# Performance work log

Hardware: AMD Instinct MI355X
Metric: run time of the kernel (lower is better)

The kernel has to match this reference:

```python
import jax, jax.numpy as jnp
import numpy as np


def setup_inputs() -> dict:
    key = jax.random.key(0)
    ks = jax.random.split(key, 8)
    B, N = 4, 256
    E, C, H = 64, 128, 256
    return {
        "edge_features": jax.random.normal(ks[0], (B, E, N, N), dtype=jnp.float32),
        "node_features": jax.random.normal(ks[1], (B, C, N), dtype=jnp.float32),
        "W1": jax.random.normal(ks[2], (H, E + 2 * C), dtype=jnp.float32) * 0.05,
        "b1": jax.random.normal(ks[3], (H,), dtype=jnp.float32) * 0.05,
        "W2": jax.random.normal(ks[4], (H, H), dtype=jnp.float32) * 0.05,
        "b2": jax.random.normal(ks[5], (H,), dtype=jnp.float32) * 0.05,
        "W3": jax.random.normal(ks[6], (1, H), dtype=jnp.float32) * 0.05,
        "b3": jax.random.normal(ks[7], (1,), dtype=jnp.float32) * 0.05,
    }


def reference(edge_features, node_features, W1, b1, W2, b2, W3, b3):
    B, C, N = node_features.shape
    # node_addon_row: [B, C, N, N] broadcast along last dim; col along dim 2
    row = jnp.broadcast_to(node_features[:, :, :, None], (B, C, N, N))
    col = jnp.broadcast_to(node_features[:, :, None, :], (B, C, N, N))
    x = jnp.concatenate([edge_features, row, col], axis=1)  # [B, E+2C, N, N]
    # 1x1 conv == channel matmul
    x = jax.nn.relu(jnp.einsum('bcnm,oc->bonm', x, W1) + b1[None, :, None, None])
    x = jax.nn.relu(jnp.einsum('bcnm,oc->bonm', x, W2) + b2[None, :, None, None])
    x = jnp.einsum('bcnm,oc->bonm', x, W3) + b3[None, :, None, None]  # [B,1,N,N]
    return x[:, 0, :, :]
```

## Files before the change

### kernel.cpp

```cpp
#include <hip/hip_runtime.h>
#include <stdint.h>

typedef __bf16 bf16x8 __attribute__((ext_vector_type(8)));
typedef __bf16 bf16x4v __attribute__((ext_vector_type(4)));
typedef float  f32x16 __attribute__((ext_vector_type(16)));
typedef float  f32x4t __attribute__((ext_vector_type(4)));
typedef unsigned int u32x2 __attribute__((ext_vector_type(2)));

#define WS_W1S 0
#define WS_W2S 32768
#define WS_R   163840
#define WS_CT  1212416

__global__ void prep_weights(const float* __restrict__ W1, const float* __restrict__ W2,
                             __bf16* __restrict__ w1s, __bf16* __restrict__ w2s) {
    int t = blockIdx.x * 256 + threadIdx.x;
    int chunk = t >> 6, lane = t & 63;
    if (chunk < 128) {
        int wid = chunk >> 5, ks = (chunk >> 1) & 15, mb = chunk & 1;
        int o = wid * 64 + mb * 32 + (lane & 31);
        int k = ks * 16 + (lane >> 5) * 8;
        const float* src = W2 + o * 256 + k;
        __bf16* dst = w2s + chunk * 512 + lane * 8;
#pragma unroll
        for (int j = 0; j < 8; ++j) dst[j] = (__bf16)src[j];
    } else if (chunk < 160) {
        int c1 = chunk - 128;
        int wid = c1 >> 3, ks = (c1 >> 1) & 3, mb = c1 & 1;
        int o = wid * 64 + mb * 32 + (lane & 31);
        int k = ks * 16 + (lane >> 5) * 8;
        const float* src = W1 + o * 320 + k;
        __bf16* dst = w1s + c1 * 512 + lane * 8;
#pragma unroll
        for (int j = 0; j < 8; ++j) dst[j] = (__bf16)src[j];
    }
}

__global__ __launch_bounds__(256) void prep_rc(
    const float* __restrict__ W1, const float* __restrict__ b1,
    const float* __restrict__ node, float* __restrict__ Rt,
    __bf16* __restrict__ Ctb) {
    __shared__ float nds[128 * 16];
    const int b = blockIdx.x >> 4, j0 = (blockIdx.x & 15) * 16;
    const int o = threadIdx.x;
    {
        int c = threadIdx.x >> 1, jh = (threadIdx.x & 1) * 8;
        const float* src = node + b * 32768 + c * 256 + j0 + jh;
        *(float4*)&nds[c * 16 + jh] = *(const float4*)src;
        *(float4*)&nds[c * 16 + jh + 4] = *(const float4*)(src + 4);
    }
    __syncthreads();
    float aR[16], aC[16];
#pragma unroll
    for (int j = 0; j < 16; ++j) { aR[j] = 0.f; aC[j] = 0.f; }
    const float* wr = W1 + o * 320 + 64;
    const float* wc = W1 + o * 320 + 192;
    for (int c4 = 0; c4 < 32; ++c4) {
        float4 wrv = *(const float4*)(wr + c4 * 4);
        float4 wcv = *(const float4*)(wc + c4 * 4);
        const float* wrp = (const float*)&wrv;
        const float* wcp = (const float*)&wcv;
#pragma unroll
        for (int r = 0; r < 4; ++r) {
            const f32x4t* nrow = (const f32x4t*)&nds[(c4 * 4 + r) * 16];
            f32x4t n0 = nrow[0], n1 = nrow[1], n2 = nrow[2], n3 = nrow[3];
#pragma unroll
            for (int q = 0; q < 4; ++q) {
                aR[q]      = fmaf(wrp[r], n0[q], aR[q]);
                aR[q + 4]  = fmaf(wrp[r], n1[q], aR[q + 4]);
                aR[q + 8]  = fmaf(wrp[r], n2[q], aR[q + 8]);
                aR[q + 12] = fmaf(wrp[r], n3[q], aR[q + 12]);
                aC[q]      = fmaf(wcp[r], n0[q], aC[q]);
                aC[q + 4]  = fmaf(wcp[r], n1[q], aC[q + 4]);
                aC[q + 8]  = fmaf(wcp[r], n2[q], aC[q + 8]);
                aC[q + 12] = fmaf(wcp[r], n3[q], aC[q + 12]);
            }
        }
    }
    float bb = b1[o];
#pragma unroll
    for (int j = 0; j < 16; ++j) {
        int idx = ((b * 256 + j0 + j) << 8) + o;
        Rt[idx] = aR[j] + bb;
        Ctb[idx] = (__bf16)aC[j];
    }
}

__device__ inline void zero_acc(f32x16 acc[2][2]) {
#pragma unroll
    for (int i = 0; i < 2; ++i)
#pragma unroll
        for (int j = 0; j < 2; ++j)
#pragma unroll
            for (int k = 0; k < 16; ++k) acc[i][j][k] = 0.f;
}

__global__ __launch_bounds__(256, 2) void fused_main(
    const float* __restrict__ edge, const __bf16* __restrict__ w1s,
    const __bf16* __restrict__ w2s, const float* __restrict__ Rt,
    const __bf16* __restrict__ Ctb, const float* __restrict__ b2,
    const float* __restrict__ W3, const float* __restrict__ b3,
    float* __restrict__ out) {
    __shared__ unsigned int lds_e[64 * 33];
    __shared__ unsigned int lds_h1[64 * 140];
    __shared__ float lds_p[64 * 9];
    __shared__ float lds_c[512];

    const int tid = threadIdx.x;
    const int wid = tid >> 6;
    const int lane = tid & 63;
    const int p31 = lane & 31;
    const int hi = lane >> 5;
    const int obase = wid * 64;

    const int blk = blockIdx.x;
    const int b   = blk >> 7;
    const int m0  = ((blk >> 5) & 3) << 6;
    const int n0  = (blk & 31) << 3;

    lds_c[tid] = b2[tid];
    lds_c[256 + tid] = W3[tid];

    const float4* eg = (const float4*)edge;
    const int a_ = tid & 15;
    const int epb = tid >> 4;
    float4 pf[4];

#define PREFETCH(nn)                                                        \
    {                                                                       \
        _Pragma("unroll")                                                   \
        for (int r = 0; r < 2; ++r) {                                       \
            int ep = r * 16 + epb;                                          \
            int f4 = (b * 64 + ep * 2) * 16384 + (nn) * 64 + (m0 >> 2) + a_;\
            pf[r * 2]     = eg[f4];                                         \
            pf[r * 2 + 1] = eg[f4 + 16384];                                 \
        }                                                                   \
    }

#define LOAD_Q(bf, q)                                                       \
    {                                                                       \
        _Pragma("unroll")                                                   \
        for (int ksl = 0; ksl < 4; ++ksl)                                   \
            _Pragma("unroll")                                               \
            for (int mb = 0; mb < 2; ++mb)                                  \
                A2q[bf][ksl][mb] = *(const bf16x8*)(w2_s +                  \
                    ((((wid << 4) + (q) * 4 + ksl) << 1) + mb) * 512 + (lane << 3)); \
    }

    PREFETCH(n0);

    bf16x4v CvR[8][2];
#pragma unroll
    for (int mb = 0; mb < 2; ++mb)
#pragma unroll
        for (int rg = 0; rg < 4; ++rg)
#pragma unroll
            for (int nb = 0; nb < 2; ++nb)
                CvR[mb * 4 + rg][nb] = *(const bf16x4v*)(Ctb +
                    ((b * 256 + m0 + nb * 32 + p31) << 8) + obase + mb * 32 + 8 * rg + 4 * hi);

    f32x16 acc[2][2];
    bf16x8 A2q[2][4][2];
    for (int it = 0; it < 8; ++it) {
        const int n = n0 + it;

        uint64_t w1a = (uint64_t)w1s;
        asm volatile("" : "+s"(w1a));
        const __bf16* w1_s = (const __bf16*)w1a;
        uint64_t w2a = (uint64_t)w2s;
        asm volatile("" : "+s"(w2a));
        const __bf16* w2_s = (const __bf16*)w2a;

#pragma unroll
        for (int r = 0; r < 2; ++r) {
            int ep = r * 16 + epb;
            const float* p0 = (const float*)&pf[r * 2];
            const float* p1 = (const float*)&pf[r * 2 + 1];
#pragma unroll
            for (int i = 0; i < 4; ++i) {
                union { __bf16 h[2]; unsigned int u; } t;
                t.h[0] = (__bf16)p0[i];
                t.h[1] = (__bf16)p1[i];
                lds_e[(a_ * 4 + i) * 33 + ep] = t.u;
            }
        }
        bf16x8 A1[2][4];
#pragma unroll
        for (int mb = 0; mb < 2; ++mb)
#pragma unroll
            for (int ks = 0; ks < 4; ++ks)
                A1[mb][ks] = *(const bf16x8*)(w1_s +
                    ((((wid << 2) + ks) << 1) + mb) * 512 + (lane << 3));
        __syncthreads();

        zero_acc(acc);
#pragma unroll
        for (int ks = 0; ks < 4; ++ks) {
            bf16x8 B1[2];
#pragma unroll
            for (int nb = 0; nb < 2; ++nb) {
                union { unsigned int u[4]; bf16x8 v; } bb;
#pragma unroll
                for (int j = 0; j < 4; ++j)
                    bb.u[j] = lds_e[(nb * 32 + p31) * 33 + ks * 8 + hi * 4 + j];
                B1[nb] = bb.v;
            }
#pragma unroll
            for (int mb = 0; mb < 2; ++mb) {
                acc[mb][0] = __builtin_amdgcn_mfma_f32_32x32x16_bf16(A1[mb][ks], B1[0], acc[mb][0], 0, 0, 0);
                acc[mb][1] = __builtin_amdgcn_mfma_f32_32x32x16_bf16(A1[mb][ks], B1[1], acc[mb][1], 0, 0, 0);
            }
        }

        const int nRow = (b * 256 + n) << 8;
#pragma unroll
        for (int mb = 0; mb < 2; ++mb) {
#pragma unroll
            for (int rg = 0; rg < 4; ++rg) {
                int och = obase + mb * 32 + 8 * rg + 4 * hi;
                f32x4t Rv = *(const f32x4t*)(Rt + nRow + och);
#pragma unroll
                for (int nb = 0; nb < 2; ++nb) {
                    int pix = nb * 32 + p31;
                    bf16x4v Cv = CvR[mb * 4 + rg][nb];
                    union { __bf16 h[4]; u32x2 u; } t;
#pragma unroll
                    for (int rr = 0; rr < 4; ++rr) {
                        float v = acc[mb][nb][rg * 4 + rr] + Rv[rr] + (float)Cv[rr];
                        t.h[rr] = (__bf16)fmaxf(v, 0.f);
                    }
                    *(u32x2*)&lds_h1[pix * 140 + (och >> 1)] = t.u;
                }
            }
        }
        LOAD_Q(0, 0);
        if (it < 7) PREFETCH(n + 1);
        __syncthreads();

        zero_acc(acc);
#pragma unroll
        for (int q = 0; q < 4; ++q) {
            if (q < 3) LOAD_Q((q + 1) & 1, q + 1);
#pragma unroll
            for (int ksl = 0; ksl < 4; ++ksl) {
                const int ksg = q * 4 + ksl;
                bf16x8 B2[2];
#pragma unroll
                for (int nb = 0; nb < 2; ++nb)
                    B2[nb] = *(const bf16x8*)&lds_h1[(nb * 32 + p31) * 140 + ksg * 8 + hi * 4];
#pragma unroll
                for (int mb = 0; mb < 2; ++mb) {
                    acc[mb][0] = __builtin_amdgcn_mfma_f32_32x32x16_bf16(A2q[q & 1][ksl][mb], B2[0], acc[mb][0], 0, 0, 0);
                    acc[mb][1] = __builtin_amdgcn_mfma_f32_32x32x16_bf16(A2q[q & 1][ksl][mb], B2[1], acc[mb][1], 0, 0, 0);
                }
            }
        }

        float part0 = 0.f, part1 = 0.f;
#pragma unroll
        for (int mb = 0; mb < 2; ++mb) {
#pragma unroll
            for (int rg = 0; rg < 4; ++rg) {
                int och = obase + mb * 32 + 8 * rg + 4 * hi;
                f32x4t b2v = *(const f32x4t*)&lds_c[och];
                f32x4t w3v = *(const f32x4t*)&lds_c[256 + och];
#pragma unroll
                for (int rr = 0; rr < 4; ++rr) {
                    float h0 = fmaxf(acc[mb][0][rg * 4 + rr] + b2v[rr], 0.f);
                    float h1v = fmaxf(acc[mb][1][rg * 4 + rr] + b2v[rr], 0.f);
                    part0 = fmaf(w3v[rr], h0, part0);
                    part1 = fmaf(w3v[rr], h1v, part1);
                }
            }
        }
        lds_p[(0 * 32 + p31) * 9 + wid * 2 + hi] = part0;
        lds_p[(1 * 32 + p31) * 9 + wid * 2 + hi] = part1;
        __syncthreads();

        if (tid < 64) {
            float s = b3[0];
#pragma unroll
            for (int k = 0; k < 8; ++k) s += lds_p[tid * 9 + k];
            out[((b * 256 + n) << 8) + m0 + tid] = s;
        }
    }
#undef PREFETCH
#undef LOAD_Q
}

extern "C" void kernel_launch(void* const* d_in, const int* in_sizes, int n_in,
                              void* d_out, int out_size, void* d_ws, size_t ws_size,
                              hipStream_t stream) {
    const float* edge = (const float*)d_in[0];
    const float* node = (const float*)d_in[1];
    const float* W1   = (const float*)d_in[2];
    const float* b1   = (const float*)d_in[3];
    const float* W2   = (const float*)d_in[4];
    const float* b2   = (const float*)d_in[5];
    const float* W3   = (const float*)d_in[6];
    const float* b3   = (const float*)d_in[7];
    char* ws = (char*)d_ws;
    __bf16* w1s = (__bf16*)(ws + WS_W1S);
    __bf16* w2s = (__bf16*)(ws + WS_W2S);
    float*  Rt  = (float*)(ws + WS_R);
    __bf16* Ctb = (__bf16*)(ws + WS_CT);

    prep_weights<<<40, 256, 0, stream>>>(W1, W2, w1s, w2s);
    prep_rc<<<64, 256, 0, stream>>>(W1, b1, node, Rt, Ctb);
    fused_main<<<512, 256, 0, stream>>>(edge, w1s, w2s, Rt, Ctb, b2, W3, b3, (float*)d_out);
}
```

Measured before the change: 160.2 us.

## Merge prep kernels, swizzle h1 LDS, hoist W1 fragments, defer output reduction

Merges the two prep kernels into one launch and writes the column term in a fragment-contiguous layout, so the main kernel loads it with coalesced lane-strided reads. The padded h1 LDS tile is replaced by an XOR-swizzled 512-byte-row layout to avoid bank conflicts while using less LDS. W1 fragments are hoisted out of the pixel loop, the per-row R vector is staged through LDS, and the final output reduction is deferred into the next iteration to drop one barrier wait. The trade-off is more live registers and an extra barrier between layers.

```diff
diff --git a/kernel.cpp b/kernel.cpp
--- a/kernel.cpp
+++ b/kernel.cpp
@@ -12,34 +12,34 @@
 #define WS_R   163840
 #define WS_CT  1212416
 
-__global__ void prep_weights(const float* __restrict__ W1, const float* __restrict__ W2,
-                             __bf16* __restrict__ w1s, __bf16* __restrict__ w2s) {
-    int t = blockIdx.x * 256 + threadIdx.x;
-    int chunk = t >> 6, lane = t & 63;
-    if (chunk < 128) {
-        int wid = chunk >> 5, ks = (chunk >> 1) & 15, mb = chunk & 1;
-        int o = wid * 64 + mb * 32 + (lane & 31);
-        int k = ks * 16 + (lane >> 5) * 8;
-        const float* src = W2 + o * 256 + k;
-        __bf16* dst = w2s + chunk * 512 + lane * 8;
-#pragma unroll
-        for (int j = 0; j < 8; ++j) dst[j] = (__bf16)src[j];
-    } else if (chunk < 160) {
-        int c1 = chunk - 128;
-        int wid = c1 >> 3, ks = (c1 >> 1) & 3, mb = c1 & 1;
-        int o = wid * 64 + mb * 32 + (lane & 31);
-        int k = ks * 16 + (lane >> 5) * 8;
-        const float* src = W1 + o * 320 + k;
-        __bf16* dst = w1s + c1 * 512 + lane * 8;
-#pragma unroll
-        for (int j = 0; j < 8; ++j) dst[j] = (__bf16)src[j];
-    }
-}
-
-__global__ __launch_bounds__(256) void prep_rc(
+__global__ __launch_bounds__(256) void prep_all(
     const float* __restrict__ W1, const float* __restrict__ b1,
-    const float* __restrict__ node, float* __restrict__ Rt,
-    __bf16* __restrict__ Ctb) {
+    const float* __restrict__ node, const float* __restrict__ W2,
+    float* __restrict__ Rt, __bf16* __restrict__ Cts,
+    __bf16* __restrict__ w1s, __bf16* __restrict__ w2s) {
+    if (blockIdx.x >= 64) {
+        int t = (blockIdx.x - 64) * 256 + threadIdx.x;
+        int chunk = t >> 6, lane = t & 63;
+        if (chunk < 128) {
+            int wid = chunk >> 5, ks = (chunk >> 1) & 15, mb = chunk & 1;
+            int o = wid * 64 + mb * 32 + (lane & 31);
+            int k = ks * 16 + (lane >> 5) * 8;
+            const float* src = W2 + o * 256 + k;
+            __bf16* dst = w2s + chunk * 512 + lane * 8;
+#pragma unroll
+            for (int j = 0; j < 8; ++j) dst[j] = (__bf16)src[j];
+        } else if (chunk < 160) {
+            int c1 = chunk - 128;
+            int wid = c1 >> 3, ks = (c1 >> 1) & 3, mb = c1 & 1;
+            int o = wid * 64 + mb * 32 + (lane & 31);
+            int k = ks * 16 + (lane >> 5) * 8;
+            const float* src = W1 + o * 320 + k;
+            __bf16* dst = w1s + c1 * 512 + lane * 8;
+#pragma unroll
+            for (int j = 0; j < 8; ++j) dst[j] = (__bf16)src[j];
+        }
+        return;
+    }
     __shared__ float nds[128 * 16];
     const int b = blockIdx.x >> 4, j0 = (blockIdx.x & 15) * 16;
     const int o = threadIdx.x;
@@ -78,33 +78,30 @@
         }
     }
     float bb = b1[o];
+    const int wid = o >> 6, mb = (o >> 5) & 1, rg = (o >> 3) & 3;
+    const int hi = (o >> 2) & 1, oq = o & 3;
 #pragma unroll
     for (int j = 0; j < 16; ++j) {
-        int idx = ((b * 256 + j0 + j) << 8) + o;
-        Rt[idx] = aR[j] + bb;
-        Ctb[idx] = (__bf16)aC[j];
-    }
-}
-
-__device__ inline void zero_acc(f32x16 acc[2][2]) {
-#pragma unroll
-    for (int i = 0; i < 2; ++i)
-#pragma unroll
-        for (int j = 0; j < 2; ++j)
-#pragma unroll
-            for (int k = 0; k < 16; ++k) acc[i][j][k] = 0.f;
+        int m = j0 + j;
+        Rt[((b * 256 + m) << 8) + o] = aR[j] + bb;
+        int mg = m >> 6, nbm = (m >> 5) & 1, p31m = m & 31;
+        int chunk = ((((b * 4 + mg) * 4 + wid) * 2 + mb) * 4 + rg) * 2 + nbm;
+        Cts[chunk * 256 + (hi * 32 + p31m) * 4 + oq] = (__bf16)aC[j];
+    }
 }
 
 __global__ __launch_bounds__(256, 2) void fused_main(
     const float* __restrict__ edge, const __bf16* __restrict__ w1s,
     const __bf16* __restrict__ w2s, const float* __restrict__ Rt,
-    const __bf16* __restrict__ Ctb, const float* __restrict__ b2,
+    const __bf16* __restrict__ Cts, const float* __restrict__ b2,
     const float* __restrict__ W3, const float* __restrict__ b3,
     float* __restrict__ out) {
     __shared__ unsigned int lds_e[64 * 33];
-    __shared__ unsigned int lds_h1[64 * 140];
+    __shared__ unsigned int lds_h1[64 * 128];
     __shared__ float lds_p[64 * 9];
     __shared__ float lds_c[512];
+    __shared__ float lds_r[256];
+    char* h1b = (char*)lds_h1;
 
     const int tid = threadIdx.x;
     const int wid = tid >> 6;
@@ -115,7 +112,8 @@
 
     const int blk = blockIdx.x;
     const int b   = blk >> 7;
-    const int m0  = ((blk >> 5) & 3) << 6;
+    const int mg  = (blk >> 5) & 3;
+    const int m0  = mg << 6;
     const int n0  = (blk & 31) << 3;
 
     lds_c[tid] = b2[tid];
@@ -149,28 +147,40 @@
 
     PREFETCH(n0);
 
-    bf16x4v CvR[8][2];
+    bf16x8 A1[2][4];
 #pragma unroll
     for (int mb = 0; mb < 2; ++mb)
 #pragma unroll
+        for (int ks = 0; ks < 4; ++ks)
+            A1[mb][ks] = *(const bf16x8*)(w1s +
+                ((((wid << 2) + ks) << 1) + mb) * 512 + (lane << 3));
+
+    bf16x4v CvR[16];
+#pragma unroll
+    for (int mb = 0; mb < 2; ++mb)
+#pragma unroll
         for (int rg = 0; rg < 4; ++rg)
 #pragma unroll
-            for (int nb = 0; nb < 2; ++nb)
-                CvR[mb * 4 + rg][nb] = *(const bf16x4v*)(Ctb +
-                    ((b * 256 + m0 + nb * 32 + p31) << 8) + obase + mb * 32 + 8 * rg + 4 * hi);
+            for (int nbm = 0; nbm < 2; ++nbm) {
+                int chunk = ((((b * 4 + mg) * 4 + wid) * 2 + mb) * 4 + rg) * 2 + nbm;
+                CvR[(mb * 4 + rg) * 2 + nbm] = *(const bf16x4v*)(Cts + chunk * 256 + lane * 4);
+            }
 
     f32x16 acc[2][2];
     bf16x8 A2q[2][4][2];
+#pragma unroll 1
     for (int it = 0; it < 8; ++it) {
         const int n = n0 + it;
 
-        uint64_t w1a = (uint64_t)w1s;
-        asm volatile("" : "+s"(w1a));
-        const __bf16* w1_s = (const __bf16*)w1a;
-        uint64_t w2a = (uint64_t)w2s;
-        asm volatile("" : "+s"(w2a));
-        const __bf16* w2_s = (const __bf16*)w2a;
-
+        if (it > 0 && tid < 64) {
+            float s = b3[0];
+#pragma unroll
+            for (int k = 0; k < 8; ++k) s += lds_p[tid * 9 + k];
+            out[((b * 256 + n - 1) << 8) + m0 + tid] = s;
+        }
+        if (tid < 64) {
+            *(f32x4t*)&lds_r[tid * 4] = *(const f32x4t*)(Rt + ((b * 256 + n) << 8) + tid * 4);
+        }
 #pragma unroll
         for (int r = 0; r < 2; ++r) {
             int ep = r * 16 + epb;
@@ -184,26 +194,24 @@
                 lds_e[(a_ * 4 + i) * 33 + ep] = t.u;
             }
         }
-        bf16x8 A1[2][4];
+        __syncthreads();
+
 #pragma unroll
         for (int mb = 0; mb < 2; ++mb)
 #pragma unroll
-            for (int ks = 0; ks < 4; ++ks)
-                A1[mb][ks] = *(const bf16x8*)(w1_s +
-                    ((((wid << 2) + ks) << 1) + mb) * 512 + (lane << 3));
-        __syncthreads();
-
-        zero_acc(acc);
+            for (int nbm = 0; nbm < 2; ++nbm)
+#pragma unroll
+                for (int k = 0; k < 16; ++k) acc[mb][nbm][k] = 0.f;
 #pragma unroll
         for (int ks = 0; ks < 4; ++ks) {
             bf16x8 B1[2];
 #pragma unroll
-            for (int nb = 0; nb < 2; ++nb) {
+            for (int nbm = 0; nbm < 2; ++nbm) {
                 union { unsigned int u[4]; bf16x8 v; } bb;
 #pragma unroll
                 for (int j = 0; j < 4; ++j)
-                    bb.u[j] = lds_e[(nb * 32 + p31) * 33 + ks * 8 + hi * 4 + j];
-                B1[nb] = bb.v;
+                    bb.u[j] = lds_e[(nbm * 32 + p31) * 33 + ks * 8 + hi * 4 + j];
+                B1[nbm] = bb.v;
             }
 #pragma unroll
             for (int mb = 0; mb < 2; ++mb) {
@@ -211,33 +219,41 @@
                 acc[mb][1] = __builtin_amdgcn_mfma_f32_32x32x16_bf16(A1[mb][ks], B1[1], acc[mb][1], 0, 0, 0);
             }
         }
-
-        const int nRow = (b * 256 + n) << 8;
 #pragma unroll
         for (int mb = 0; mb < 2; ++mb) {
 #pragma unroll
             for (int rg = 0; rg < 4; ++rg) {
                 int och = obase + mb * 32 + 8 * rg + 4 * hi;
-                f32x4t Rv = *(const f32x4t*)(Rt + nRow + och);
-#pragma unroll
-                for (int nb = 0; nb < 2; ++nb) {
-                    int pix = nb * 32 + p31;
-                    bf16x4v Cv = CvR[mb * 4 + rg][nb];
+                f32x4t Rv = *(const f32x4t*)&lds_r[och];
+                int col16 = (wid << 3) + (mb << 2) + rg;
+#pragma unroll
+                for (int nbm = 0; nbm < 2; ++nbm) {
+                    int p = nbm * 32 + p31;
+                    bf16x4v Cv = CvR[(mb * 4 + rg) * 2 + nbm];
                     union { __bf16 h[4]; u32x2 u; } t;
 #pragma unroll
                     for (int rr = 0; rr < 4; ++rr) {
-                        float v = acc[mb][nb][rg * 4 + rr] + Rv[rr] + (float)Cv[rr];
+                        float v = acc[mb][nbm][rg * 4 + rr] + Rv[rr] + (float)Cv[rr];
                         t.h[rr] = (__bf16)fmaxf(v, 0.f);
                     }
-                    *(u32x2*)&lds_h1[pix * 140 + (och >> 1)] = t.u;
+                    *(u32x2*)(h1b + p * 512 + ((col16 ^ p31) << 4) + (hi << 3)) = t.u;
                 }
             }
         }
+        __syncthreads();
+
+        uint64_t w2a = (uint64_t)w2s;
+        asm volatile("" : "+s"(w2a));
+        const __bf16* w2_s = (const __bf16*)w2a;
+        if (it < 7) PREFETCH(n + 1);
         LOAD_Q(0, 0);
-        if (it < 7) PREFETCH(n + 1);
-        __syncthreads();
-
-        zero_acc(acc);
+
+#pragma unroll
+        for (int mb = 0; mb < 2; ++mb)
+#pragma unroll
+            for (int nbm = 0; nbm < 2; ++nbm)
+#pragma unroll
+                for (int k = 0; k < 16; ++k) acc[mb][nbm][k] = 0.f;
 #pragma unroll
         for (int q = 0; q < 4; ++q) {
             if (q < 3) LOAD_Q((q + 1) & 1, q + 1);
@@ -246,8 +262,11 @@
                 const int ksg = q * 4 + ksl;
                 bf16x8 B2[2];
 #pragma unroll
-                for (int nb = 0; nb < 2; ++nb)
-                    B2[nb] = *(const bf16x8*)&lds_h1[(nb * 32 + p31) * 140 + ksg * 8 + hi * 4];
+                for (int nbm = 0; nbm < 2; ++nbm) {
+                    int p = nbm * 32 + p31;
+                    B2[nbm] = *(const bf16x8*)(h1b + p * 512 +
+                              ((((ksg << 1) + hi) ^ p31) << 4));
+                }
 #pragma unroll
                 for (int mb = 0; mb < 2; ++mb) {
                     acc[mb][0] = __builtin_amdgcn_mfma_f32_32x32x16_bf16(A2q[q & 1][ksl][mb], B2[0], acc[mb][0], 0, 0, 0);
@@ -276,13 +295,13 @@
         lds_p[(0 * 32 + p31) * 9 + wid * 2 + hi] = part0;
         lds_p[(1 * 32 + p31) * 9 + wid * 2 + hi] = part1;
         __syncthreads();
-
-        if (tid < 64) {
-            float s = b3[0];
-#pragma unroll
-            for (int k = 0; k < 8; ++k) s += lds_p[tid * 9 + k];
-            out[((b * 256 + n) << 8) + m0 + tid] = s;
-        }
+    }
+
+    if (tid < 64) {
+        float s = b3[0];
+#pragma unroll
+        for (int k = 0; k < 8; ++k) s += lds_p[tid * 9 + k];
+        out[((b * 256 + n0 + 7) << 8) + m0 + tid] = s;
     }
 #undef PREFETCH
 #undef LOAD_Q
@@ -303,9 +322,8 @@
     __bf16* w1s = (__bf16*)(ws + WS_W1S);
     __bf16* w2s = (__bf16*)(ws + WS_W2S);
     float*  Rt  = (float*)(ws + WS_R);
-    __bf16* Ctb = (__bf16*)(ws + WS_CT);
-
-    prep_weights<<<40, 256, 0, stream>>>(W1, W2, w1s, w2s);
-    prep_rc<<<64, 256, 0, stream>>>(W1, b1, node, Rt, Ctb);
-    fused_main<<<512, 256, 0, stream>>>(edge, w1s, w2s, Rt, Ctb, b2, W3, b3, (float*)d_out);
+    __bf16* Cts = (__bf16*)(ws + WS_CT);
+
+    prep_all<<<104, 256, 0, stream>>>(W1, b1, node, W2, Rt, Cts, w1s, w2s);
+    fused_main<<<512, 256, 0, stream>>>(edge, w1s, w2s, Rt, Cts, b2, W3, b3, (float*)d_out);
 }
```

Result: slower. 204.0 us (+27.3%).
